# Performance work log

Hardware: AMD Instinct MI355X
Metric: run time of the kernel (lower is better)

Reference implementation:

```python
import jax, jax.numpy as jnp
import numpy as np

W1 = 1.0
W2 = 1.0


def setup_inputs() -> dict:
    key = jax.random.key(0)
    k1, k2 = jax.random.split(key)
    points1 = jax.random.normal(k1, (8, 4096, 3), dtype=jnp.float32)
    points2 = jax.random.normal(k2, (8, 4096, 3), dtype=jnp.float32)
    return {"points1": points1, "points2": points2}


def reference(points1, points2):
    # Pairwise squared L2 distances: [B, N1, N2].
    # (torch code does sqrt(dist)**2 which is mathematically identity for dist>=0.)
    diff = points1[:, :, None, :] - points2[:, None, :, :]  # [B, N1, N2, 3]
    dist = jnp.sum(diff * diff, axis=3)                      # [B, N1, N2]
    dist_min1 = jnp.min(dist, axis=2)  # nearest in points2 for each points1: [B, N1]
    dist_min2 = jnp.min(dist, axis=1)  # nearest in points1 for each points2: [B, N2]
    loss1 = dist_min1.mean(axis=1)     # [B]
    loss2 = dist_min2.mean(axis=1)     # [B]
    loss = W1 * loss1 + W2 * loss2
    return loss.mean()  # each_batch=False
```

## Files before the change

### kernel.cpp

```cpp
#include <hip/hip_runtime.h>
#include <float.h>


typedef float v2f __attribute__((ext_vector_type(2)));

#define NBATCH 8
#define NPTS   4096
#define BLK    256
#define PTS    16
#define NCHUNK 32
#define CHUNK  (NPTS / NCHUNK)
#define PAIRS  (CHUNK / 2)

__global__ __launch_bounds__(BLK)
void chamfer_min_kernel(const float* __restrict__ p1,
                        const float* __restrict__ p2,
                        unsigned int* __restrict__ mins )
{
    __shared__ float4 sXY[PAIRS];
    __shared__ float4 sZW[PAIRS];

    int bid   = blockIdx.x;
    int chunk = bid & (NCHUNK - 1);  bid >>= 5;
    int b     = bid & (NBATCH - 1);  bid >>= 3;
    int dir   = bid;

    const float* A    = dir ? p2 : p1;
    const float* Bpts = dir ? p1 : p2;
    int tid = threadIdx.x;

    if (tid < PAIRS) {
        const float* s = Bpts + ((size_t)b * NPTS + chunk * CHUNK + 2 * tid) * 3;
        float x0 = s[0], y0 = s[1], z0 = s[2];
        float x1 = s[3], y1 = s[4], z1 = s[5];
        sXY[tid] = make_float4(x0, x1, y0, y1);
        sZW[tid] = make_float4(z0, z1,
                               x0 * x0 + y0 * y0 + z0 * z0,
                               x1 * x1 + y1 * y1 + z1 * z1);
    }

    v2f  m2x[PTS], m2y[PTS], m2z[PTS];
    float n1[PTS], bestE[PTS], bestO[PTS];
#pragma unroll
    for (int k = 0; k < PTS; ++k) {
        const float* s = A + ((size_t)b * NPTS + tid + k * BLK) * 3;
        float x = s[0], y = s[1], z = s[2];
        float mx = -2.0f * x, my = -2.0f * y, mz = -2.0f * z;
        m2x[k] = (v2f){mx, mx};
        m2y[k] = (v2f){my, my};
        m2z[k] = (v2f){mz, mz};
        n1[k]  = x * x + y * y + z * z;
        bestE[k] = FLT_MAX;
        bestO[k] = FLT_MAX;
    }
    __syncthreads();

#pragma unroll 2
    for (int p = 0; p < PAIRS; ++p) {
        float4 xy = sXY[p];
        float4 zw = sZW[p];
        v2f qx = (v2f){xy.x, xy.y};
        v2f qy = (v2f){xy.z, xy.w};
        v2f qz = (v2f){zw.x, zw.y};
        v2f qw = (v2f){zw.z, zw.w};
#pragma unroll
        for (int k = 0; k < PTS; ++k) {
            v2f t = __builtin_elementwise_fma(m2x[k], qx, qw);
            t = __builtin_elementwise_fma(m2y[k], qy, t);
            t = __builtin_elementwise_fma(m2z[k], qz, t);
            bestE[k] = fminf(bestE[k], t.x);
            bestO[k] = fminf(bestO[k], t.y);
        }
    }

    unsigned int* marr = mins + ((size_t)dir * NBATCH + b) * NPTS + tid;
#pragma unroll
    for (int k = 0; k < PTS; ++k) {
        float d = fmaxf(fminf(bestE[k], bestO[k]) + n1[k], 0.0f);
        atomicMin(&marr[k * BLK], __float_as_uint(d));
    }
}

__global__ __launch_bounds__(1024)
void chamfer_reduce_kernel(const float* __restrict__ mins, float* __restrict__ out)
{
    __shared__ float wave_sums[16];
    const float4* m4 = (const float4*)mins;
    float s = 0.0f;
#pragma unroll
    for (int i = 0; i < 16; ++i) {
        float4 v = m4[threadIdx.x + i * 1024];
        s += (v.x + v.y) + (v.z + v.w);
    }
#pragma unroll
    for (int off = 32; off > 0; off >>= 1)
        s += __shfl_down(s, off, 64);
    int wave = threadIdx.x >> 6;
    if ((threadIdx.x & 63) == 0) wave_sums[wave] = s;
    __syncthreads();
    if (threadIdx.x < 16) {
        s = wave_sums[threadIdx.x];
#pragma unroll
        for (int off = 8; off > 0; off >>= 1)
            s += __shfl_down(s, off, 16);
        if (threadIdx.x == 0) out[0] = s / (float)(NBATCH * NPTS);
    }
}

extern "C" void kernel_launch(void* const* d_in, const int* in_sizes, int n_in,
                              void* d_out, int out_size, void* d_ws, size_t ws_size,
                              hipStream_t stream) {
    const float* p1 = (const float*)d_in[0];
    const float* p2 = (const float*)d_in[1];
    float* out = (float*)d_out;
    unsigned int* mins = (unsigned int*)d_ws;

    hipMemsetAsync(d_ws, 0xFF, (size_t)2 * NBATCH * NPTS * sizeof(unsigned int), stream);

    int nblocks = 2 * NBATCH * NCHUNK;
    chamfer_min_kernel<<<nblocks, BLK, 0, stream>>>(p1, p2, mins);
    chamfer_reduce_kernel<<<1, 1024, 0, stream>>>((const float*)d_ws, out);
}
```

Baseline: 81.09 us.

## Replace atomicMin with per-split partial buffers and parallel min-sum reduction

```diff
diff --git a/kernel.cpp b/kernel.cpp
--- a/kernel.cpp
+++ b/kernel.cpp
@@ -8,31 +8,32 @@
 #define NPTS   4096
 #define BLK    256
 #define PTS    16
-#define NCHUNK 32
-#define CHUNK  (NPTS / NCHUNK)
-#define PAIRS  (CHUNK / 2)
+#define SSPLIT 32
+#define BCHUNK (NPTS / SSPLIT)
+#define PAIRS  (BCHUNK / 2)
+#define NSLOTS (2 * NBATCH * NPTS)
 
 __global__ __launch_bounds__(BLK)
 void chamfer_min_kernel(const float* __restrict__ p1,
                         const float* __restrict__ p2,
-                        unsigned int* __restrict__ mins )
+                        float* __restrict__ parts )
 {
     __shared__ float4 sXY[PAIRS];
     __shared__ float4 sZW[PAIRS];
 
-    int bid   = blockIdx.x;
-    int chunk = bid & (NCHUNK - 1);  bid >>= 5;
-    int b     = bid & (NBATCH - 1);  bid >>= 3;
-    int dir   = bid;
+    int bid = blockIdx.x;
+    int s   = bid & (SSPLIT - 1);  bid >>= 5;
+    int b   = bid & (NBATCH - 1);  bid >>= 3;
+    int dir = bid;
 
     const float* A    = dir ? p2 : p1;
     const float* Bpts = dir ? p1 : p2;
     int tid = threadIdx.x;
 
     if (tid < PAIRS) {
-        const float* s = Bpts + ((size_t)b * NPTS + chunk * CHUNK + 2 * tid) * 3;
-        float x0 = s[0], y0 = s[1], z0 = s[2];
-        float x1 = s[3], y1 = s[4], z1 = s[5];
+        const float* src = Bpts + ((size_t)b * NPTS + s * BCHUNK + 2 * tid) * 3;
+        float x0 = src[0], y0 = src[1], z0 = src[2];
+        float x1 = src[3], y1 = src[4], z1 = src[5];
         sXY[tid] = make_float4(x0, x1, y0, y1);
         sZW[tid] = make_float4(z0, z1,
                                x0 * x0 + y0 * y0 + z0 * z0,
@@ -40,18 +41,17 @@
     }
 
     v2f  m2x[PTS], m2y[PTS], m2z[PTS];
-    float n1[PTS], bestE[PTS], bestO[PTS];
+    float n1[PTS], best[PTS];
 #pragma unroll
     for (int k = 0; k < PTS; ++k) {
-        const float* s = A + ((size_t)b * NPTS + tid + k * BLK) * 3;
-        float x = s[0], y = s[1], z = s[2];
+        const float* src = A + ((size_t)b * NPTS + tid + k * BLK) * 3;
+        float x = src[0], y = src[1], z = src[2];
         float mx = -2.0f * x, my = -2.0f * y, mz = -2.0f * z;
         m2x[k] = (v2f){mx, mx};
         m2y[k] = (v2f){my, my};
         m2z[k] = (v2f){mz, mz};
         n1[k]  = x * x + y * y + z * z;
-        bestE[k] = FLT_MAX;
-        bestO[k] = FLT_MAX;
+        best[k] = FLT_MAX;
     }
     __syncthreads();
 
@@ -68,43 +68,39 @@
             v2f t = __builtin_elementwise_fma(m2x[k], qx, qw);
             t = __builtin_elementwise_fma(m2y[k], qy, t);
             t = __builtin_elementwise_fma(m2z[k], qz, t);
-            bestE[k] = fminf(bestE[k], t.x);
-            bestO[k] = fminf(bestO[k], t.y);
+            best[k] = fminf(best[k], fminf(t.x, t.y));
         }
     }
 
-    unsigned int* marr = mins + ((size_t)dir * NBATCH + b) * NPTS + tid;
+    float* dst = parts + (size_t)s * NSLOTS + ((size_t)dir * NBATCH + b) * NPTS + tid;
 #pragma unroll
-    for (int k = 0; k < PTS; ++k) {
-        float d = fmaxf(fminf(bestE[k], bestO[k]) + n1[k], 0.0f);
-        atomicMin(&marr[k * BLK], __float_as_uint(d));
-    }
+    for (int k = 0; k < PTS; ++k)
+        dst[k * BLK] = fmaxf(best[k] + n1[k], 0.0f);
 }
 
-__global__ __launch_bounds__(1024)
-void chamfer_reduce_kernel(const float* __restrict__ mins, float* __restrict__ out)
+__global__ __launch_bounds__(BLK)
+void chamfer_reduce_kernel(const float* __restrict__ parts, float* __restrict__ out)
 {
-    __shared__ float wave_sums[16];
-    const float4* m4 = (const float4*)mins;
-    float s = 0.0f;
+    int j = blockIdx.x * BLK + threadIdx.x;
+    float m0 = FLT_MAX, m1 = FLT_MAX, m2 = FLT_MAX, m3 = FLT_MAX;
 #pragma unroll
-    for (int i = 0; i < 16; ++i) {
-        float4 v = m4[threadIdx.x + i * 1024];
-        s += (v.x + v.y) + (v.z + v.w);
+    for (int s = 0; s < SSPLIT; s += 4) {
+        m0 = fminf(m0, parts[(size_t)(s + 0) * NSLOTS + j]);
+        m1 = fminf(m1, parts[(size_t)(s + 1) * NSLOTS + j]);
+        m2 = fminf(m2, parts[(size_t)(s + 2) * NSLOTS + j]);
+        m3 = fminf(m3, parts[(size_t)(s + 3) * NSLOTS + j]);
     }
+    float v = fminf(fminf(m0, m1), fminf(m2, m3));
 #pragma unroll
     for (int off = 32; off > 0; off >>= 1)
-        s += __shfl_down(s, off, 64);
+        v += __shfl_down(v, off, 64);
+    __shared__ float wsum[4];
     int wave = threadIdx.x >> 6;
-    if ((threadIdx.x & 63) == 0) wave_sums[wave] = s;
+    if ((threadIdx.x & 63) == 0) wsum[wave] = v;
     __syncthreads();
-    if (threadIdx.x < 16) {
-        s = wave_sums[threadIdx.x];
-#pragma unroll
-        for (int off = 8; off > 0; off >>= 1)
-            s += __shfl_down(s, off, 16);
-        if (threadIdx.x == 0) out[0] = s / (float)(NBATCH * NPTS);
-    }
+    if (threadIdx.x == 0)
+        atomicAdd(out, (wsum[0] + wsum[1] + wsum[2] + wsum[3]) *
+                       (1.0f / (float)(NBATCH * NPTS)));
 }
 
 extern "C" void kernel_launch(void* const* d_in, const int* in_sizes, int n_in,
@@ -113,11 +109,11 @@
     const float* p1 = (const float*)d_in[0];
     const float* p2 = (const float*)d_in[1];
     float* out = (float*)d_out;
-    unsigned int* mins = (unsigned int*)d_ws;
+    float* parts = (float*)d_ws;
 
-    hipMemsetAsync(d_ws, 0xFF, (size_t)2 * NBATCH * NPTS * sizeof(unsigned int), stream);
+    hipMemsetAsync(d_out, 0, sizeof(float), stream);
 
-    int nblocks = 2 * NBATCH * NCHUNK;
-    chamfer_min_kernel<<<nblocks, BLK, 0, stream>>>(p1, p2, mins);
-    chamfer_reduce_kernel<<<1, 1024, 0, stream>>>((const float*)d_ws, out);
+    int nblocks = 2 * NBATCH * SSPLIT;
+    chamfer_min_kernel<<<nblocks, BLK, 0, stream>>>(p1, p2, parts);
+    chamfer_reduce_kernel<<<NSLOTS / BLK, BLK, 0, stream>>>(parts, out);
 }
```

Result: slower. 86.17 us (+6.3%).
